# Performance work log

Hardware: AMD Instinct MI355X
Metric: run time of the kernel (lower is better)

Reference implementation:

```python
import jax, jax.numpy as jnp
import numpy as np

VOCAB = 50000
PAD = VOCAB - 1          # self.pad = vocab - 1
EDIM = 128
WFEAT = 128
LABELS = 2
SLOPE = 0.0
B, N = 64, 512


def setup_inputs() -> dict:
    key = jax.random.key(0)
    ks = jax.random.split(key, 8)
    # padded token ids, variable lengths in [N//2, N]
    doc = jax.random.randint(ks[0], (B, N), 0, VOCAB - 1, dtype=jnp.int32)
    lengths = jax.random.randint(ks[1], (B,), N // 2, N + 1)
    doc = jnp.where(jnp.arange(N)[None, :] < lengths[:, None], doc, PAD).astype(jnp.int32)
    emb = jax.random.normal(ks[2], (VOCAB, EDIM), jnp.float32) * 0.1      # nn.Embedding weight
    W = jax.random.normal(ks[3], (EDIM, WFEAT), jnp.float32) * 0.05      # GAT linear
    a_src = jax.random.normal(ks[4], (WFEAT,), jnp.float32) * 0.05        # attention vec (src half)
    a_dst = jax.random.normal(ks[5], (WFEAT,), jnp.float32) * 0.05        # attention vec (dst half)
    Wc = jax.random.normal(ks[6], (WFEAT, LABELS), jnp.float32) * 0.05    # classifier
    bc = jnp.zeros((LABELS,), jnp.float32)
    return {"doc": doc, "emb": emb, "W": W, "a_src": a_src, "a_dst": a_dst, "Wc": Wc, "bc": bc}


def _build_adj(doc):
    # Vectorized replacement of the python loop over (doc==pad).nonzero():
    # for each pad position d: adj[b, d, :, :] = 0 ; adj[b, :, d, :] = -1
    pad = doc == PAD                               # [B, N]
    row = pad[:, :, None]                          # query i padded
    col = pad[:, None, :]                          # key   j padded
    i = jnp.arange(N)[:, None]
    j = jnp.arange(N)[None, :]
    both = jnp.where(j > i, -1.0, 0.0)             # [N, N]
    adj = jnp.where(row & ~col, 0.0,
          jnp.where(col & ~row, -1.0,
          jnp.where(row & col, both, 1.0)))        # [B, N, N]
    return adj


def reference(doc, emb, W, a_src, a_dst, Wc, bc):
    adj = _build_adj(doc)                          # [B, N, N]
    words = emb[doc]                               # [B, N, E]
    # --- GATLayerBatchEnabled (canonical batched GAT) ---
    h = jnp.einsum('bne,ef->bnf', words, W)        # [B, N, F]
    e_src = h @ a_src                              # [B, N]
    e_dst = h @ a_dst                              # [B, N]
    e = jax.nn.leaky_relu(e_src[:, :, None] + e_dst[:, None, :], negative_slope=SLOPE)
    e = jnp.where(adj > 0, e, -1e9)                # mask non-edges / pads
    attention = jax.nn.softmax(e, axis=-1)         # [B, N, N]
    sentence = jax.nn.elu(jnp.einsum('bij,bjf->bif', attention, h))  # [B, N, F]
    # --- pooling + classifier ---
    poolSentence = jnp.mean(sentence, axis=1)      # [B, F]
    label = jax.nn.softmax(poolSentence @ Wc + bc, axis=0)  # softmax over dim=0 per source
    return (poolSentence, attention, sentence, label)
```

## Files before the change

kernel.cpp:

```cpp
#include <hip/hip_runtime.h>

#define NB 64
#define NN 512
#define ED 128
#define NF 128
#define PAD_ID 49999

typedef unsigned short ushort_t;
typedef __attribute__((ext_vector_type(8))) short short8v;
typedef __attribute__((ext_vector_type(4))) float f32x4;

__device__ __forceinline__ unsigned short f2b(float f) {
    unsigned int u = __float_as_uint(f);
    u = (u + 0x7fffu + ((u >> 16) & 1u)) >> 16;
    return (unsigned short)u;
}
__device__ __forceinline__ float b2f(unsigned short h) {
    return __uint_as_float(((unsigned int)h) << 16);
}

__global__ __launch_bounds__(256) void k_h(
    const int* __restrict__ doc, const float* __restrict__ emb,
    const float* __restrict__ W, const float* __restrict__ a_src,
    const float* __restrict__ a_dst, ushort_t* __restrict__ hT,
    float* __restrict__ esrc, float* __restrict__ edst)
{
    __shared__ float wl[32][128];
    const int tid = threadIdx.x;
    const int t0  = blockIdx.x * 32;
    const int b   = t0 >> 9;
    const int tl0 = t0 & (NN - 1);

#pragma unroll
    for (int k = 0; k < 4; ++k) {
        int idx = tid + k * 256;
        int tok = idx >> 5;
        int e4  = (idx & 31) << 2;
        int d   = doc[t0 + tok];
        *(float4*)&wl[tok][e4] = *(const float4*)(emb + (size_t)d * ED + e4);
    }
    __syncthreads();

    const int fg = tid & 31;  const int f0 = fg << 2;
    const int tg = tid >> 5;

    float acc[4][4] = {};
    for (int e = 0; e < 128; e += 4) {
        float4 wr[4];
#pragma unroll
        for (int k = 0; k < 4; ++k)
            wr[k] = *(const float4*)(W + (e + k) * NF + f0);
#pragma unroll
        for (int r = 0; r < 4; ++r) {
            const float4 x = *(const float4*)&wl[tg * 4 + r][e];
            const float xa[4] = {x.x, x.y, x.z, x.w};
#pragma unroll
            for (int k = 0; k < 4; ++k) {
                acc[r][0] = fmaf(xa[k], wr[k].x, acc[r][0]);
                acc[r][1] = fmaf(xa[k], wr[k].y, acc[r][1]);
                acc[r][2] = fmaf(xa[k], wr[k].z, acc[r][2]);
                acc[r][3] = fmaf(xa[k], wr[k].w, acc[r][3]);
            }
        }
    }

    const float4 as = *(const float4*)(a_src + f0);
    const float4 ad = *(const float4*)(a_dst + f0);
#pragma unroll
    for (int r = 0; r < 4; ++r) {
        float es = acc[r][0]*as.x + acc[r][1]*as.y + acc[r][2]*as.z + acc[r][3]*as.w;
        float ed = acc[r][0]*ad.x + acc[r][1]*ad.y + acc[r][2]*ad.z + acc[r][3]*ad.w;
#pragma unroll
        for (int off = 1; off < 32; off <<= 1) {
            es += __shfl_xor(es, off);
            ed += __shfl_xor(ed, off);
        }
        if (fg == 0) {
            esrc[t0 + tg * 4 + r] = es;
            edst[t0 + tg * 4 + r] = ed;
        }
    }

#pragma unroll
    for (int c = 0; c < 4; ++c) {
        union { ushort_t u[4]; uint2 v; } pk;
#pragma unroll
        for (int r = 0; r < 4; ++r) pk.u[r] = f2b(acc[r][c]);
        *(uint2*)(hT + (size_t)b * NF * NN + (size_t)(f0 + c) * NN + tl0 + tg * 4) = pk.v;
    }
}

__global__ __launch_bounds__(256, 4) void k_attn(
    const int* __restrict__ doc, const ushort_t* __restrict__ hT,
    const float* __restrict__ esrc, const float* __restrict__ edst,
    float* __restrict__ out_att, float* __restrict__ out_sent,
    float* __restrict__ pool)
{
    __shared__ float edl[NN];
    __shared__ float esl[32], rvl[32], invl[32];
    __shared__ ushort_t p_l[32][520];

    const int tid = threadIdx.x;
    const int b   = blockIdx.y;
    const int i0  = blockIdx.x * 32;

#pragma unroll
    for (int k = 0; k < 2; ++k) {
        int j = tid + k * 256;
        edl[j] = (doc[b * NN + j] == PAD_ID) ? -3e30f : edst[b * NN + j];
    }
    if (tid < 32) {
        esl[tid] = esrc[b * NN + i0 + tid];
        rvl[tid] = (doc[b * NN + i0 + tid] == PAD_ID) ? 0.f : 1.f;
    }
    __syncthreads();

    const int w    = tid >> 6;
    const int lane = tid & 63;

    {
        const int rl  = lane & 7;
        const int kg  = lane >> 3;
        const int row = w * 8 + rl;
        const float es = esl[row];
        const bool  rv = rvl[row] != 0.f;

        float m = -1e30f;
#pragma unroll
        for (int ks = 0; ks < 8; ++ks) {
            const int j0 = kg * 8 + ks * 64;
            const float4 e0 = *(const float4*)&edl[j0], e1 = *(const float4*)&edl[j0 + 4];
            m = fmaxf(m, fmaxf(fmaxf(fmaxf(es+e0.x,es+e0.y),fmaxf(es+e0.z,es+e0.w)),
                               fmaxf(fmaxf(es+e1.x,es+e1.y),fmaxf(es+e1.z,es+e1.w))));
        }
        m = fmaxf(m, 0.f);
        m = fmaxf(m, __shfl_xor(m, 8));
        m = fmaxf(m, __shfl_xor(m, 16));
        m = fmaxf(m, __shfl_xor(m, 32));

        float s = 0.f;
#pragma unroll
        for (int ks = 0; ks < 8; ++ks) {
            const int j0 = kg * 8 + ks * 64;
            const float4 e0 = *(const float4*)&edl[j0], e1 = *(const float4*)&edl[j0 + 4];
            const float xs[8] = {es+e0.x, es+e0.y, es+e0.z, es+e0.w,
                                 es+e1.x, es+e1.y, es+e1.z, es+e1.w};
            float p[8];
#pragma unroll
            for (int q = 0; q < 8; ++q) {
                float pv;
                if (rv) pv = (xs[q] > -1e20f) ? __expf(fmaxf(xs[q], 0.f) - m) : 0.f;
                else    pv = 1.f;
                p[q] = pv; s += pv;
            }
            union { unsigned int u[4]; uint4 v; } pk;
#pragma unroll
            for (int q = 0; q < 4; ++q)
                pk.u[q] = ((unsigned)f2b(p[2*q+1]) << 16) | (unsigned)f2b(p[2*q]);
            *(uint4*)&p_l[row][j0] = pk.v;
        }
        s += __shfl_xor(s, 8);
        s += __shfl_xor(s, 16);
        s += __shfl_xor(s, 32);
        if (kg == 0) invl[row] = rv ? (1.f / s) : (1.f / 512.f);
    }
    __syncthreads();

#pragma unroll
    for (int r8 = 0; r8 < 8; ++r8) {
        const int r = w * 8 + r8;
        const float inv = invl[r];
        float* arow = out_att + ((size_t)(b * NN + i0 + r)) * NN;
#pragma unroll
        for (int half = 0; half < 2; ++half) {
            const uint2 v = *(const uint2*)&p_l[r][half * 256 + lane * 4];
            float4 o;
            o.x = b2f((ushort_t)(v.x & 0xffff)) * inv;
            o.y = b2f((ushort_t)(v.x >> 16))    * inv;
            o.z = b2f((ushort_t)(v.y & 0xffff)) * inv;
            o.w = b2f((ushort_t)(v.y >> 16))    * inv;
            *(float4*)(arow + half * 256 + lane * 4) = o;
        }
    }

    const int mr  = lane & 15;
    const int grp = lane >> 4;
    const int rt  = w & 1;
    const int fh  = w >> 1;

    short8v a_regs[16];
#pragma unroll
    for (int ks = 0; ks < 16; ++ks)
        a_regs[ks] = *(const short8v*)&p_l[rt * 16 + mr][grp * 8 + ks * 32];

    const ushort_t* hTb = hT + (size_t)b * NF * NN;
#pragma unroll
    for (int t = 0; t < 4; ++t) {
        const int n0 = (fh * 4 + t) * 16;
        f32x4 acc = {0.f, 0.f, 0.f, 0.f};
        const ushort_t* bp = hTb + (size_t)(n0 + mr) * NN + grp * 8;
#pragma unroll
        for (int ks = 0; ks < 16; ++ks) {
            const short8v bv = *(const short8v*)(bp + ks * 32);
            acc = __builtin_amdgcn_mfma_f32_16x16x32_bf16(a_regs[ks], bv, acc, 0, 0, 0);
        }
        const int feat = n0 + mr;
        float psum = 0.f;
#pragma unroll
        for (int reg = 0; reg < 4; ++reg) {
            const int rl2 = rt * 16 + grp * 4 + reg;
            float v = acc[reg] * invl[rl2];
            v = v > 0.f ? v : expm1f(v);
            out_sent[((size_t)(b * NN + i0 + rl2)) * NF + feat] = v;
            psum += v;
        }
        psum += __shfl_xor(psum, 16);
        psum += __shfl_xor(psum, 32);
        if (lane < 16) atomicAdd(&pool[b * NF + feat], psum);
    }
}

__global__ __launch_bounds__(128) void k_label(
    const float* __restrict__ poolAccum, const float* __restrict__ Wc,
    const float* __restrict__ bc, float* __restrict__ out_pool,
    float* __restrict__ out_label)
{
    __shared__ float wc0[NF], wc1[NF];
    const int tid = threadIdx.x;
    if (tid < NF) { wc0[tid] = Wc[tid * 2]; wc1[tid] = Wc[tid * 2 + 1]; }
    __syncthreads();

    for (int i = tid; i < NB * NF / 4; i += 128) {
        float4 v = *(const float4*)(poolAccum + i * 4);
        v.x *= (1.f/512.f); v.y *= (1.f/512.f); v.z *= (1.f/512.f); v.w *= (1.f/512.f);
        *(float4*)(out_pool + i * 4) = v;
    }

    const int b = tid & 63, c = tid >> 6;
    const float* pbp = poolAccum + b * NF;
    const float* wcp = c ? wc1 : wc0;
    float z = bc[c];
    for (int f = 0; f < NF; f += 4) {
        const float4 pv = *(const float4*)(pbp + f);
        z = fmaf(pv.x * (1.f/512.f), wcp[f + 0], z);
        z = fmaf(pv.y * (1.f/512.f), wcp[f + 1], z);
        z = fmaf(pv.z * (1.f/512.f), wcp[f + 2], z);
        z = fmaf(pv.w * (1.f/512.f), wcp[f + 3], z);
    }
    float mz = z;
#pragma unroll
    for (int off = 32; off; off >>= 1) mz = fmaxf(mz, __shfl_xor(mz, off));
    float e = __expf(z - mz);
    float sv = e;
#pragma unroll
    for (int off = 32; off; off >>= 1) sv += __shfl_xor(sv, off);
    out_label[b * 2 + c] = e / sv;
}

extern "C" void kernel_launch(void* const* d_in, const int* in_sizes, int n_in,
                              void* d_out, int out_size, void* d_ws, size_t ws_size,
                              hipStream_t stream)
{
    const int*   doc   = (const int*)d_in[0];
    const float* emb   = (const float*)d_in[1];
    const float* W     = (const float*)d_in[2];
    const float* a_src = (const float*)d_in[3];
    const float* a_dst = (const float*)d_in[4];
    const float* Wc    = (const float*)d_in[5];
    const float* bc    = (const float*)d_in[6];

    float* out       = (float*)d_out;
    float* out_pool  = out;
    float* out_att   = out_pool + NB * NF;
    float* out_sent  = out_att + (size_t)NB * NN * NN;
    float* out_label = out_sent + (size_t)NB * NN * NF;

    char* base = (char*)d_ws;
    ushort_t* hT  = (ushort_t*)base;
    float* esrc   = (float*)(base + (size_t)NB * NF * NN * 2);
    float* edst   = esrc + NB * NN;
    float* pool   = edst + NB * NN;

    hipMemsetAsync(pool, 0, NB * NF * sizeof(float), stream);

    k_h<<<(NB * NN) / 32, 256, 0, stream>>>(doc, emb, W, a_src, a_dst, hT, esrc, edst);

    dim3 g2(NN / 32, NB);
    k_attn<<<g2, 256, 0, stream>>>(doc, hT, esrc, edst, out_att, out_sent, pool);

    k_label<<<1, 128, 0, stream>>>(pool, Wc, bc, out_pool, out_label);
}
```

Measured before the change: 174.5 us.

## Halve attention row tile to 16 and fold pool zeroing into k_h

The attention kernel now processes 16 query rows per block instead of 32. That doubles the grid, shrinks shared memory, and raises the launch-bounds occupancy hint from 4 to 8. The MFMA stage drops the register-cached A operand and reads it from LDS on each k-step, with each wave covering two 16-feature tiles. The separate hipMemsetAsync for the pool accumulator is replaced by zeroing inside the first 8 blocks of k_h, which removes one launch. The trade-off is that each block re-reads the full hT slab and edst for half as many rows, doubling that traffic.

```diff
diff --git a/kernel.cpp b/kernel.cpp
--- a/kernel.cpp
+++ b/kernel.cpp
@@ -23,13 +23,19 @@
     const int* __restrict__ doc, const float* __restrict__ emb,
     const float* __restrict__ W, const float* __restrict__ a_src,
     const float* __restrict__ a_dst, ushort_t* __restrict__ hT,
-    float* __restrict__ esrc, float* __restrict__ edst)
+    float* __restrict__ esrc, float* __restrict__ edst,
+    float* __restrict__ pool)
 {
     __shared__ float wl[32][128];
     const int tid = threadIdx.x;
     const int t0  = blockIdx.x * 32;
     const int b   = t0 >> 9;
     const int tl0 = t0 & (NN - 1);
+
+    if (blockIdx.x < 8) {
+        const float4 z4 = make_float4(0.f, 0.f, 0.f, 0.f);
+        *(float4*)(pool + blockIdx.x * 1024 + tid * 4) = z4;
+    }
 
 #pragma unroll
     for (int k = 0; k < 4; ++k) {
@@ -90,26 +96,26 @@
     }
 }
 
-__global__ __launch_bounds__(256, 4) void k_attn(
+__global__ __launch_bounds__(256, 8) void k_attn(
     const int* __restrict__ doc, const ushort_t* __restrict__ hT,
     const float* __restrict__ esrc, const float* __restrict__ edst,
     float* __restrict__ out_att, float* __restrict__ out_sent,
     float* __restrict__ pool)
 {
     __shared__ float edl[NN];
-    __shared__ float esl[32], rvl[32], invl[32];
-    __shared__ ushort_t p_l[32][520];
+    __shared__ float esl[16], rvl[16], invl[16];
+    __shared__ ushort_t p_l[16][520];
 
     const int tid = threadIdx.x;
     const int b   = blockIdx.y;
-    const int i0  = blockIdx.x * 32;
+    const int i0  = blockIdx.x * 16;
 
 #pragma unroll
     for (int k = 0; k < 2; ++k) {
         int j = tid + k * 256;
         edl[j] = (doc[b * NN + j] == PAD_ID) ? -3e30f : edst[b * NN + j];
     }
-    if (tid < 32) {
+    if (tid < 16) {
         esl[tid] = esrc[b * NN + i0 + tid];
         rvl[tid] = (doc[b * NN + i0 + tid] == PAD_ID) ? 0.f : 1.f;
     }
@@ -119,29 +125,30 @@
     const int lane = tid & 63;
 
     {
-        const int rl  = lane & 7;
-        const int kg  = lane >> 3;
-        const int row = w * 8 + rl;
+        const int rl  = lane & 3;
+        const int kg  = lane >> 2;
+        const int row = w * 4 + rl;
         const float es = esl[row];
         const bool  rv = rvl[row] != 0.f;
 
         float m = -1e30f;
 #pragma unroll
-        for (int ks = 0; ks < 8; ++ks) {
-            const int j0 = kg * 8 + ks * 64;
+        for (int ks = 0; ks < 4; ++ks) {
+            const int j0 = kg * 8 + ks * 128;
             const float4 e0 = *(const float4*)&edl[j0], e1 = *(const float4*)&edl[j0 + 4];
             m = fmaxf(m, fmaxf(fmaxf(fmaxf(es+e0.x,es+e0.y),fmaxf(es+e0.z,es+e0.w)),
                                fmaxf(fmaxf(es+e1.x,es+e1.y),fmaxf(es+e1.z,es+e1.w))));
         }
         m = fmaxf(m, 0.f);
+        m = fmaxf(m, __shfl_xor(m, 4));
         m = fmaxf(m, __shfl_xor(m, 8));
         m = fmaxf(m, __shfl_xor(m, 16));
         m = fmaxf(m, __shfl_xor(m, 32));
 
         float s = 0.f;
 #pragma unroll
-        for (int ks = 0; ks < 8; ++ks) {
-            const int j0 = kg * 8 + ks * 64;
+        for (int ks = 0; ks < 4; ++ks) {
+            const int j0 = kg * 8 + ks * 128;
             const float4 e0 = *(const float4*)&edl[j0], e1 = *(const float4*)&edl[j0 + 4];
             const float xs[8] = {es+e0.x, es+e0.y, es+e0.z, es+e0.w,
                                  es+e1.x, es+e1.y, es+e1.z, es+e1.w};
@@ -159,6 +166,7 @@
                 pk.u[q] = ((unsigned)f2b(p[2*q+1]) << 16) | (unsigned)f2b(p[2*q]);
             *(uint4*)&p_l[row][j0] = pk.v;
         }
+        s += __shfl_xor(s, 4);
         s += __shfl_xor(s, 8);
         s += __shfl_xor(s, 16);
         s += __shfl_xor(s, 32);
@@ -167,8 +175,8 @@
     __syncthreads();
 
 #pragma unroll
-    for (int r8 = 0; r8 < 8; ++r8) {
-        const int r = w * 8 + r8;
+    for (int r4 = 0; r4 < 4; ++r4) {
+        const int r = w * 4 + r4;
         const float inv = invl[r];
         float* arow = out_att + ((size_t)(b * NN + i0 + r)) * NN;
 #pragma unroll
@@ -185,30 +193,25 @@
 
     const int mr  = lane & 15;
     const int grp = lane >> 4;
-    const int rt  = w & 1;
-    const int fh  = w >> 1;
-
-    short8v a_regs[16];
-#pragma unroll
-    for (int ks = 0; ks < 16; ++ks)
-        a_regs[ks] = *(const short8v*)&p_l[rt * 16 + mr][grp * 8 + ks * 32];
 
     const ushort_t* hTb = hT + (size_t)b * NF * NN;
-#pragma unroll
-    for (int t = 0; t < 4; ++t) {
-        const int n0 = (fh * 4 + t) * 16;
+    const ushort_t* ap  = &p_l[mr][grp * 8];
+#pragma unroll
+    for (int t = 0; t < 2; ++t) {
+        const int n0 = (w * 2 + t) * 16;
         f32x4 acc = {0.f, 0.f, 0.f, 0.f};
         const ushort_t* bp = hTb + (size_t)(n0 + mr) * NN + grp * 8;
 #pragma unroll
         for (int ks = 0; ks < 16; ++ks) {
+            const short8v av = *(const short8v*)(ap + ks * 32);
             const short8v bv = *(const short8v*)(bp + ks * 32);
-            acc = __builtin_amdgcn_mfma_f32_16x16x32_bf16(a_regs[ks], bv, acc, 0, 0, 0);
+            acc = __builtin_amdgcn_mfma_f32_16x16x32_bf16(av, bv, acc, 0, 0, 0);
         }
         const int feat = n0 + mr;
         float psum = 0.f;
 #pragma unroll
         for (int reg = 0; reg < 4; ++reg) {
-            const int rl2 = rt * 16 + grp * 4 + reg;
+            const int rl2 = grp * 4 + reg;
             float v = acc[reg] * invl[rl2];
             v = v > 0.f ? v : expm1f(v);
             out_sent[((size_t)(b * NN + i0 + rl2)) * NF + feat] = v;
@@ -281,11 +284,9 @@
     float* edst   = esrc + NB * NN;
     float* pool   = edst + NB * NN;
 
-    hipMemsetAsync(pool, 0, NB * NF * sizeof(float), stream);
-
-    k_h<<<(NB * NN) / 32, 256, 0, stream>>>(doc, emb, W, a_src, a_dst, hT, esrc, edst);
-
-    dim3 g2(NN / 32, NB);
+    k_h<<<(NB * NN) / 32, 256, 0, stream>>>(doc, emb, W, a_src, a_dst, hT, esrc, edst, pool);
+
+    dim3 g2(NN / 16, NB);
     k_attn<<<g2, 256, 0, stream>>>(doc, hT, esrc, edst, out_att, out_sent, pool);
 
     k_label<<<1, 128, 0, stream>>>(pool, Wc, bc, out_pool, out_label);
```

New measurement: 190.4 us. +9.1%, slower.
